# Performance work log

Hardware: AMD Instinct MI355X
Metric: run time of the kernel (lower is better)

Reference implementation:

```python
import jax, jax.numpy as jnp
import numpy as np

H, HD = 16, 64
DIM = H * HD
ROT_DIM = 64
ROT_BASE = 10000.0
B, MAXLEN = 4, 2048
SEQLENS = [2048, 1536, 1024, 512]


def setup_inputs() -> dict:
    key = jax.random.key(0)
    k1, k2, k3 = jax.random.split(key, 3)
    total = sum(SEQLENS)
    hidden_states = jax.random.normal(k1, (total, DIM), jnp.float32)
    Wqkv_w = jax.random.normal(k2, (3 * DIM, DIM), jnp.float32) * (DIM ** -0.5)
    Wo_w = jax.random.normal(k3, (DIM, DIM), jnp.float32) * (DIM ** -0.5)
    cu = np.cumsum([0] + SEQLENS).astype(np.int32)
    idx = np.concatenate([b * MAXLEN + np.arange(L) for b, L in enumerate(SEQLENS)]).astype(np.int64)
    mask = np.zeros((B, MAXLEN), np.int32)
    for b, L in enumerate(SEQLENS):
        mask[b, :L] = 1
    return {"hidden_states": hidden_states, "Wqkv_w": Wqkv_w, "Wo_w": Wo_w,
            "cu_seqlens": jnp.asarray(cu), "indices": jnp.asarray(idx),
            "attn_mask": jnp.asarray(mask), "max_seqlen": MAXLEN}


def _rope(x, positions):
    # x: (B, S, H, D). Non-interleaved (rotate-half) RoPE over first ROT_DIM dims,
    # matching flash_attn RotaryEmbedding(interleaved=False, scale_base=None).
    d2 = ROT_DIM // 2
    inv_freq = 1.0 / (ROT_BASE ** (jnp.arange(0, ROT_DIM, 2, dtype=jnp.float32) / ROT_DIM))
    freqs = positions[:, None].astype(jnp.float32) * inv_freq[None, :]  # (S, d2)
    cos = jnp.cos(freqs)[None, :, None, :]
    sin = jnp.sin(freqs)[None, :, None, :]
    x1, x2 = x[..., :d2], x[..., d2:ROT_DIM]
    rot = jnp.concatenate([x1 * cos - x2 * sin, x2 * cos + x1 * sin], axis=-1)
    if ROT_DIM < x.shape[-1]:
        rot = jnp.concatenate([rot, x[..., ROT_DIM:]], axis=-1)
    return rot


def reference(hidden_states, Wqkv_w, Wo_w, cu_seqlens, indices, attn_mask, max_seqlen):
    # QKV projection on unpadded tokens (no bias: attn_qkv_bias=False)
    qkv = hidden_states @ Wqkv_w.T  # (nnz, 3*dim)
    # pad_input: scatter tokens into (B*max_seqlen) padded layout
    padded = jnp.zeros((B * max_seqlen, 3 * DIM), qkv.dtype).at[indices].set(qkv)
    qkv = padded.reshape(B, max_seqlen, 3, H, HD)
    pos = jnp.arange(max_seqlen)
    q = _rope(qkv[:, :, 0], pos)  # (B, S, H, HD)
    k = _rope(qkv[:, :, 1], pos)
    v = qkv[:, :, 2]
    # SDPA (no attn_mask, matching the source's non-flash path; p_dropout=0)
    scale = 1.0 / jnp.sqrt(jnp.float32(HD))
    scores = jnp.einsum('bqhd,bkhd->bhqk', q, k) * scale  # (B, H, S, S)
    probs = jax.nn.softmax(scores, axis=-1)
    attn = jnp.einsum('bhqk,bkhd->bqhd', probs, v).reshape(B * max_seqlen, DIM)
    # unpad_input_only: gather valid tokens back
    attn = attn[indices]  # (nnz, dim)
    return attn @ Wo_w.T  # attn_out_bias=False, out_drop=Identity
```

## Files before the change

### kernel.cpp

```cpp
#include <hip/hip_runtime.h>
#include <math.h>

#define NH 16
#define HD 64
#define DIM 1024
#define QKV_DIM 3072
#define MAXLEN 2048
#define TOTAL 5120

typedef unsigned short ushort_t;
typedef unsigned int uint_t;
typedef __attribute__((ext_vector_type(8))) short bf16x8;
typedef __attribute__((ext_vector_type(8))) unsigned short ushort8;
typedef __attribute__((ext_vector_type(4))) float f32x4;

__device__ __constant__ int g_cu[5]  = {0, 2048, 3584, 4608, 5120};
__device__ __constant__ int g_seq[4] = {2048, 1536, 1024, 512};

__device__ inline ushort_t f2bf(float f) {
    uint_t u = __float_as_uint(f);
    uint_t r = u + 0x7FFFu + ((u >> 16) & 1u);
    return (ushort_t)(r >> 16);
}
__device__ inline float bf2f(ushort_t h) { return __uint_as_float(((uint_t)h) << 16); }

__global__ __launch_bounds__(256) void split_bf16(const float* __restrict__ x,
                                                  ushort_t* __restrict__ hi,
                                                  ushort_t* __restrict__ lo, int n4) {
    int i = blockIdx.x * 256 + threadIdx.x;
    if (i >= n4) return;
    float4 v = ((const float4*)x)[i];
    ushort_t h0 = f2bf(v.x), h1 = f2bf(v.y), h2 = f2bf(v.z), h3 = f2bf(v.w);
    ushort_t l0 = f2bf(v.x - bf2f(h0));
    ushort_t l1 = f2bf(v.y - bf2f(h1));
    ushort_t l2 = f2bf(v.z - bf2f(h2));
    ushort_t l3 = f2bf(v.w - bf2f(h3));
    ushort4 hv = {h0, h1, h2, h3};
    ushort4 lv = {l0, l1, l2, l3};
    ((ushort4*)hi)[i] = hv;
    ((ushort4*)lo)[i] = lv;
}

__global__ __launch_bounds__(256) void gemm_mfma_split(
    const ushort_t* __restrict__ Ah, const ushort_t* __restrict__ Al,
    const ushort_t* __restrict__ Bh, const ushort_t* __restrict__ Bl,
    float* __restrict__ C, int M, int N, int K) {
    __shared__ ushort_t sAh[128 * 32], sAl[128 * 32];
    __shared__ ushort_t sBh[128 * 32], sBl[128 * 32];

    const int tid = threadIdx.x;
    const int lane = tid & 63;
    const int w = tid >> 6;
    const int bm = blockIdx.y * 128, bn = blockIdx.x * 128;
    const int wm = (w >> 1) * 64, wn = (w & 1) * 64;

    f32x4 acc[4][4] = {};

    const int srow = tid >> 2;
    const int scol = (tid & 3) * 8;

    for (int k0 = 0; k0 < K; k0 += 32) {
        __syncthreads();
#pragma unroll
        for (int i = 0; i < 2; ++i) {
            int r = i * 64 + srow;
            size_t ga = (size_t)(bm + r) * K + k0 + scol;
            size_t gb = (size_t)(bn + r) * K + k0 + scol;
            int ls = r * 32 + scol;
            *(ushort8*)&sAh[ls] = *(const ushort8*)&Ah[ga];
            *(ushort8*)&sAl[ls] = *(const ushort8*)&Al[ga];
            *(ushort8*)&sBh[ls] = *(const ushort8*)&Bh[gb];
            *(ushort8*)&sBl[ls] = *(const ushort8*)&Bl[gb];
        }
        __syncthreads();

        const int frow = lane & 15;
        const int fk = (lane >> 4) * 8;
        bf16x8 ah[4], al[4], bh[4], bl[4];
#pragma unroll
        for (int t = 0; t < 4; ++t) {
            int ar = (wm + t * 16 + frow) * 32 + fk;
            int br = (wn + t * 16 + frow) * 32 + fk;
            ah[t] = *(const bf16x8*)&sAh[ar];
            al[t] = *(const bf16x8*)&sAl[ar];
            bh[t] = *(const bf16x8*)&sBh[br];
            bl[t] = *(const bf16x8*)&sBl[br];
        }
#pragma unroll
        for (int mt = 0; mt < 4; ++mt)
#pragma unroll
            for (int nt = 0; nt < 4; ++nt) {
                acc[mt][nt] = __builtin_amdgcn_mfma_f32_16x16x32_bf16(ah[mt], bh[nt], acc[mt][nt], 0, 0, 0);
                acc[mt][nt] = __builtin_amdgcn_mfma_f32_16x16x32_bf16(ah[mt], bl[nt], acc[mt][nt], 0, 0, 0);
                acc[mt][nt] = __builtin_amdgcn_mfma_f32_16x16x32_bf16(al[mt], bh[nt], acc[mt][nt], 0, 0, 0);
            }
    }

    const int crow0 = (lane >> 4) * 4;
    const int ccol = lane & 15;
#pragma unroll
    for (int mt = 0; mt < 4; ++mt)
#pragma unroll
        for (int nt = 0; nt < 4; ++nt) {
            size_t rbase = (size_t)(bm + wm + mt * 16 + crow0) * N + bn + wn + nt * 16 + ccol;
#pragma unroll
            for (int r = 0; r < 4; ++r)
                C[rbase + (size_t)r * N] = acc[mt][nt][r];
        }
}

__global__ __launch_bounds__(256) void rope_split_kv(
    const float* __restrict__ qkv,
    ushort_t* __restrict__ kh, ushort_t* __restrict__ kl,
    ushort_t* __restrict__ vth, ushort_t* __restrict__ vtl) {
    __shared__ float tv[64][65];

    const int tiles_pref[5] = {0, 32, 56, 72, 80};
    int t = blockIdx.x;
    int b = 0;
    while (t >= tiles_pref[b + 1]) b++;
    const int t0 = (t - tiles_pref[b]) * 64;
    const int base = g_cu[b];
    const int h = blockIdx.y;
    const int tid = threadIdx.x;

    {
        int r = tid >> 2, jg = tid & 3;
        int tok = base + t0 + r;
        const float* kp = qkv + (size_t)tok * QKV_DIM + DIM + h * HD;
        float x1[8], x2[8];
        *(float4*)&x1[0] = *(const float4*)&kp[8 * jg + 0];
        *(float4*)&x1[4] = *(const float4*)&kp[8 * jg + 4];
        *(float4*)&x2[0] = *(const float4*)&kp[32 + 8 * jg + 0];
        *(float4*)&x2[4] = *(const float4*)&kp[32 + 8 * jg + 4];
        float pos = (float)(t0 + r);
        ushort8 h0v, l0v, h1v, l1v;
#pragma unroll
        for (int jj = 0; jj < 8; ++jj) {
            int j = 8 * jg + jj;
            float invf = powf(10000.0f, -(float)j / 32.0f);
            float sn, cs;
            sincosf(pos * invf, &sn, &cs);
            float y0 = x1[jj] * cs - x2[jj] * sn;
            float y1 = x2[jj] * cs + x1[jj] * sn;
            ushort_t hh = f2bf(y0);
            h0v[jj] = hh; l0v[jj] = f2bf(y0 - bf2f(hh));
            hh = f2bf(y1);
            h1v[jj] = hh; l1v[jj] = f2bf(y1 - bf2f(hh));
        }
        size_t o0 = (size_t)tok * DIM + h * HD + 8 * jg;
        *(ushort8*)&kh[o0] = h0v;      *(ushort8*)&kh[o0 + 32] = h1v;
        *(ushort8*)&kl[o0] = l0v;      *(ushort8*)&kl[o0 + 32] = l1v;
    }

#pragma unroll
    for (int it = 0; it < 4; ++it) {
        int item = tid + it * 256;
        int r = item >> 4, c4 = item & 15;
        *(float4*)&tv[r][c4 * 4] =
            *(const float4*)(qkv + (size_t)(base + t0 + r) * QKV_DIM + 2 * DIM + h * HD + c4 * 4);
    }
    __syncthreads();
#pragma unroll
    for (int it = 0; it < 2; ++it) {
        int chunk = tid + it * 256;
        int dd = chunk >> 3, tb = chunk & 7;
        ushort8 vh, vl;
#pragma unroll
        for (int i = 0; i < 8; ++i) {
            float f = tv[tb * 8 + i][dd];
            ushort_t hh = f2bf(f);
            vh[i] = hh; vl[i] = f2bf(f - bf2f(hh));
        }
        size_t off = (size_t)(h * HD + dd) * TOTAL + base + t0 + tb * 8;
        *(ushort8*)&vth[off] = vh;
        *(ushort8*)&vtl[off] = vl;
    }
}

__global__ __launch_bounds__(256) void attn_mfma(
    const float* __restrict__ qkv,
    const ushort_t* __restrict__ kh, const ushort_t* __restrict__ kl,
    const ushort_t* __restrict__ vth, const ushort_t* __restrict__ vtl,
    float* __restrict__ attnb) {
    __shared__ ushort_t sKh[64 * 64], sKl[64 * 64];
    __shared__ ushort_t sVh[64 * 64], sVl[64 * 64];
    __shared__ ushort_t sPh[4][16 * 72], sPl[4][16 * 72];

    const int tiles_pref[5] = {0, 32, 56, 72, 80};
    int t = blockIdx.x;
    int b = 0;
    while (t >= tiles_pref[b + 1]) b++;
    const int qstart = (t - tiles_pref[b]) * 64;
    const int h = blockIdx.y;
    const int L = g_seq[b];
    const int base = g_cu[b];
    const int tid = threadIdx.x;
    const int lane = tid & 63;
    const int w = tid >> 6;
    const int c = lane & 15;
    const int g = lane >> 4;

    const float SCALE = 0.125f * 1.44269504088896f;
    const int qrow = qstart + 16 * w + c;
    const float* qp = qkv + (size_t)(base + qrow) * QKV_DIM + h * HD;
    float x1[8], x2[8];
    *(float4*)&x1[0] = *(const float4*)&qp[8 * g + 0];
    *(float4*)&x1[4] = *(const float4*)&qp[8 * g + 4];
    *(float4*)&x2[0] = *(const float4*)&qp[32 + 8 * g + 0];
    *(float4*)&x2[4] = *(const float4*)&qp[32 + 8 * g + 4];
    bf16x8 qh0, ql0, qh1, ql1;
#pragma unroll
    for (int jj = 0; jj < 8; ++jj) {
        int j = 8 * g + jj;
        float invf = powf(10000.0f, -(float)j / 32.0f);
        float sn, cs;
        sincosf((float)qrow * invf, &sn, &cs);
        float y0 = (x1[jj] * cs - x2[jj] * sn) * SCALE;
        float y1 = (x2[jj] * cs + x1[jj] * sn) * SCALE;
        ushort_t hh = f2bf(y0);
        qh0[jj] = (short)hh; ql0[jj] = (short)f2bf(y0 - bf2f(hh));
        hh = f2bf(y1);
        qh1[jj] = (short)hh; ql1[jj] = (short)f2bf(y1 - bf2f(hh));
    }

    f32x4 o[4] = {};
    float m[4] = {-1e30f, -1e30f, -1e30f, -1e30f};
    float d[4] = {};

    const int ntiles = L >> 6;
    for (int kt = 0; kt < ntiles; ++kt) {
        const int k0 = kt << 6;
        __syncthreads();
#pragma unroll
        for (int it = 0; it < 8; ++it) {
            int chunk = it * 64 + lane;
            int r = chunk >> 3, s = chunk & 7;
            int gb = s ^ (r & 7);
            if (w < 2) {
                const ushort_t* src = (w == 0 ? kh : kl) +
                    (size_t)(base + k0 + r) * DIM + h * HD + 8 * gb;
                ushort8 v = *(const ushort8*)src;
                *(ushort8*)((w == 0 ? sKh : sKl) + r * 64 + 8 * s) = v;
            } else {
                const ushort_t* src = (w == 2 ? vth : vtl) +
                    (size_t)(h * HD + r) * TOTAL + base + k0 + 8 * gb;
                ushort8 v = *(const ushort8*)src;
                *(ushort8*)((w == 2 ? sVh : sVl) + r * 64 + 8 * s) = v;
            }
        }
        __syncthreads();

        f32x4 sf[4] = {};
#pragma unroll
        for (int f = 0; f < 4; ++f) {
#pragma unroll
            for (int ks = 0; ks < 2; ++ks) {
                int off = (16 * f + c) * 64 + 8 * ((4 * ks + g) ^ (c & 7));
                bf16x8 bh = *(const bf16x8*)&sKh[off];
                bf16x8 bl = *(const bf16x8*)&sKl[off];
                bf16x8 qh = ks ? qh1 : qh0;
                bf16x8 ql = ks ? ql1 : ql0;
                sf[f] = __builtin_amdgcn_mfma_f32_16x16x32_bf16(qh, bh, sf[f], 0, 0, 0);
                sf[f] = __builtin_amdgcn_mfma_f32_16x16x32_bf16(qh, bl, sf[f], 0, 0, 0);
                sf[f] = __builtin_amdgcn_mfma_f32_16x16x32_bf16(ql, bh, sf[f], 0, 0, 0);
            }
        }

#pragma unroll
        for (int r = 0; r < 4; ++r) {
            float rm = fmaxf(fmaxf(sf[0][r], sf[1][r]), fmaxf(sf[2][r], sf[3][r]));
            rm = fmaxf(rm, __shfl_xor(rm, 1));
            rm = fmaxf(rm, __shfl_xor(rm, 2));
            rm = fmaxf(rm, __shfl_xor(rm, 4));
            rm = fmaxf(rm, __shfl_xor(rm, 8));
            float mn = fmaxf(m[r], rm);
            float corr = exp2f(m[r] - mn);
            m[r] = mn;
            float p0 = exp2f(sf[0][r] - mn);
            float p1 = exp2f(sf[1][r] - mn);
            float p2 = exp2f(sf[2][r] - mn);
            float p3 = exp2f(sf[3][r] - mn);
            float ps = (p0 + p1) + (p2 + p3);
            ps += __shfl_xor(ps, 1);
            ps += __shfl_xor(ps, 2);
            ps += __shfl_xor(ps, 4);
            ps += __shfl_xor(ps, 8);
            d[r] = d[r] * corr + ps;
            o[0][r] *= corr; o[1][r] *= corr; o[2][r] *= corr; o[3][r] *= corr;
            int ro = (4 * g + r) * 72 + c;
            ushort_t ph;
            ph = f2bf(p0); sPh[w][ro +  0] = ph; sPl[w][ro +  0] = f2bf(p0 - bf2f(ph));
            ph = f2bf(p1); sPh[w][ro + 16] = ph; sPl[w][ro + 16] = f2bf(p1 - bf2f(ph));
            ph = f2bf(p2); sPh[w][ro + 32] = ph; sPl[w][ro + 32] = f2bf(p2 - bf2f(ph));
            ph = f2bf(p3); sPh[w][ro + 48] = ph; sPl[w][ro + 48] = f2bf(p3 - bf2f(ph));
        }
        asm volatile("s_waitcnt lgkmcnt(0)" ::: "memory");
        __builtin_amdgcn_sched_barrier(0);

#pragma unroll
        for (int ks = 0; ks < 2; ++ks) {
            bf16x8 pah = *(const bf16x8*)&sPh[w][c * 72 + 32 * ks + 8 * g];
            bf16x8 pal = *(const bf16x8*)&sPl[w][c * 72 + 32 * ks + 8 * g];
#pragma unroll
            for (int fd = 0; fd < 4; ++fd) {
                int off = (16 * fd + c) * 64 + 8 * ((4 * ks + g) ^ (c & 7));
                bf16x8 vh = *(const bf16x8*)&sVh[off];
                bf16x8 vl = *(const bf16x8*)&sVl[off];
                o[fd] = __builtin_amdgcn_mfma_f32_16x16x32_bf16(pah, vh, o[fd], 0, 0, 0);
                o[fd] = __builtin_amdgcn_mfma_f32_16x16x32_bf16(pah, vl, o[fd], 0, 0, 0);
                o[fd] = __builtin_amdgcn_mfma_f32_16x16x32_bf16(pal, vh, o[fd], 0, 0, 0);
            }
        }
    }

    const int npad = MAXLEN - L;
#pragma unroll
    for (int r = 0; r < 4; ++r) {
        float dr = d[r];
        if (npad) dr += (float)npad * exp2f(0.0f - m[r]);
        float inv = 1.0f / dr;
        int row = base + qstart + 16 * w + 4 * g + r;
        float* op = attnb + (size_t)row * DIM + h * HD;
#pragma unroll
        for (int fd = 0; fd < 4; ++fd)
            op[16 * fd + c] = o[fd][r] * inv;
    }
}

extern "C" void kernel_launch(void* const* d_in, const int* in_sizes, int n_in,
                              void* d_out, int out_size, void* d_ws, size_t ws_size,
                              hipStream_t stream) {
    const float* hidden = (const float*)d_in[0];
    const float* Wqkv = (const float*)d_in[1];
    const float* Wo = (const float*)d_in[2];
    float* out = (float*)d_out;

    const int total = in_sizes[0] / DIM;

    float* qkv = (float*)d_ws;
    float* attnb = qkv + (size_t)total * QKV_DIM;
    ushort_t* us = (ushort_t*)(attnb + (size_t)total * DIM);
    const size_t nh = (size_t)total * DIM;
    const size_t nw = (size_t)QKV_DIM * DIM;
    const size_t no = (size_t)DIM * DIM;
    ushort_t* h_hi = us;            ushort_t* h_lo = h_hi + nh;
    ushort_t* wq_hi = h_lo + nh;    ushort_t* wq_lo = wq_hi + nw;
    ushort_t* ao_hi = wq_lo + nw;   ushort_t* ao_lo = ao_hi + nh;
    ushort_t* wo_hi = ao_lo + nh;   ushort_t* wo_lo = wo_hi + no;
    ushort_t* kh  = h_hi;
    ushort_t* kl  = h_lo;
    ushort_t* vth = wq_hi;
    ushort_t* vtl = ao_hi;

    split_bf16<<<(int)(nh / 4 + 255) / 256, 256, 0, stream>>>(hidden, h_hi, h_lo, (int)(nh / 4));
    split_bf16<<<(int)(nw / 4 + 255) / 256, 256, 0, stream>>>(Wqkv, wq_hi, wq_lo, (int)(nw / 4));
    split_bf16<<<(int)(no / 4 + 255) / 256, 256, 0, stream>>>(Wo, wo_hi, wo_lo, (int)(no / 4));

    gemm_mfma_split<<<dim3(QKV_DIM / 128, total / 128), 256, 0, stream>>>(
        h_hi, h_lo, wq_hi, wq_lo, qkv, total, QKV_DIM, DIM);

    rope_split_kv<<<dim3(80, NH), 256, 0, stream>>>(qkv, kh, kl, vth, vtl);

    attn_mfma<<<dim3(80, NH), 256, 0, stream>>>(qkv, kh, kl, vth, vtl, attnb);

    split_bf16<<<(int)(nh / 4 + 255) / 256, 256, 0, stream>>>(attnb, ao_hi, ao_lo, (int)(nh / 4));
    gemm_mfma_split<<<dim3(DIM / 128, total / 128), 256, 0, stream>>>(
        ao_hi, ao_lo, wo_hi, wo_lo, out, total, DIM, DIM);
}
```

Baseline: 580.5 us.

## Restructure attention kernel: 128-row tiles, register prefetch, lazy rescale, swizzled P

The attention kernel now uses 512-thread blocks covering 128 query rows, so each K/V tile loaded into shared memory is reused by twice as many waves. Next-tile K/V loads are prefetched into registers while the current tile is computed, and all eight waves share the staging work. Softmax skips the max/rescale step unless the row max grows by more than a threshold, and row sums are kept per lane and reduced once at the end. The P scratch buffer is XOR-swizzled instead of padded, and block IDs are remapped across heads. This adds register pressure and a looser numeric bound on the deferred max.

Measured after the change: 707.3 us. +21.8%, slower.

```diff
diff --git a/kernel.cpp b/kernel.cpp
--- a/kernel.cpp
+++ b/kernel.cpp
@@ -178,28 +178,39 @@
     }
 }
 
-__global__ __launch_bounds__(256) void attn_mfma(
+__global__ __launch_bounds__(512, 4) void attn_mfma(
     const float* __restrict__ qkv,
     const ushort_t* __restrict__ kh, const ushort_t* __restrict__ kl,
     const ushort_t* __restrict__ vth, const ushort_t* __restrict__ vtl,
     float* __restrict__ attnb) {
     __shared__ ushort_t sKh[64 * 64], sKl[64 * 64];
     __shared__ ushort_t sVh[64 * 64], sVl[64 * 64];
-    __shared__ ushort_t sPh[4][16 * 72], sPl[4][16 * 72];
-
-    const int tiles_pref[5] = {0, 32, 56, 72, 80};
-    int t = blockIdx.x;
+    __shared__ ushort_t sPh[8][16 * 64], sPl[8][16 * 64];
+
+    int fid = blockIdx.x;
+    fid = (fid & 7) * 80 + (fid >> 3);
+    const int h = fid / 40;
+    int t = fid % 40;
+    const int tiles_pref[5] = {0, 16, 28, 36, 40};
     int b = 0;
     while (t >= tiles_pref[b + 1]) b++;
-    const int qstart = (t - tiles_pref[b]) * 64;
-    const int h = blockIdx.y;
+    const int qstart = (t - tiles_pref[b]) * 128;
     const int L = g_seq[b];
     const int base = g_cu[b];
+
     const int tid = threadIdx.x;
     const int lane = tid & 63;
     const int w = tid >> 6;
     const int c = lane & 15;
     const int g = lane >> 4;
+
+    const int arr = w >> 1;
+    const int half = w & 1;
+    const int l3 = lane >> 3;
+    const int sl = lane & 7;
+    const int gb = sl ^ l3;
+    const ushort_t* gsrc = arr == 0 ? kh : arr == 1 ? kl : arr == 2 ? vth : vtl;
+    ushort_t* ldst = arr == 0 ? sKh : arr == 1 ? sKl : arr == 2 ? sVh : sVl;
 
     const float SCALE = 0.125f * 1.44269504088896f;
     const int qrow = qstart + 16 * w + c;
@@ -226,30 +237,38 @@
 
     f32x4 o[4] = {};
     float m[4] = {-1e30f, -1e30f, -1e30f, -1e30f};
-    float d[4] = {};
+    float dp[4] = {};
+    ushort8 pre[4];
 
     const int ntiles = L >> 6;
+#pragma unroll
+    for (int it = 0; it < 4; ++it) {
+        int rr = half * 32 + it * 8 + l3;
+        size_t src = (arr < 2) ? ((size_t)(base + rr) * DIM + h * HD + 8 * gb)
+                               : ((size_t)(h * HD + rr) * TOTAL + base + 8 * gb);
+        pre[it] = *(const ushort8*)&gsrc[src];
+    }
+
     for (int kt = 0; kt < ntiles; ++kt) {
-        const int k0 = kt << 6;
         __syncthreads();
 #pragma unroll
-        for (int it = 0; it < 8; ++it) {
-            int chunk = it * 64 + lane;
-            int r = chunk >> 3, s = chunk & 7;
-            int gb = s ^ (r & 7);
-            if (w < 2) {
-                const ushort_t* src = (w == 0 ? kh : kl) +
-                    (size_t)(base + k0 + r) * DIM + h * HD + 8 * gb;
-                ushort8 v = *(const ushort8*)src;
-                *(ushort8*)((w == 0 ? sKh : sKl) + r * 64 + 8 * s) = v;
-            } else {
-                const ushort_t* src = (w == 2 ? vth : vtl) +
-                    (size_t)(h * HD + r) * TOTAL + base + k0 + 8 * gb;
-                ushort8 v = *(const ushort8*)src;
-                *(ushort8*)((w == 2 ? sVh : sVl) + r * 64 + 8 * s) = v;
-            }
+        for (int it = 0; it < 4; ++it) {
+            int rr = half * 32 + it * 8 + l3;
+            *(ushort8*)&ldst[rr * 64 + 8 * sl] = pre[it];
         }
         __syncthreads();
+
+        if (kt + 1 < ntiles) {
+            const int k1 = (kt + 1) << 6;
+#pragma unroll
+            for (int it = 0; it < 4; ++it) {
+                int rr = half * 32 + it * 8 + l3;
+                size_t src = (arr < 2)
+                    ? ((size_t)(base + k1 + rr) * DIM + h * HD + 8 * gb)
+                    : ((size_t)(h * HD + rr) * TOTAL + base + k1 + 8 * gb);
+                pre[it] = *(const ushort8*)&gsrc[src];
+            }
+        }
 
         f32x4 sf[4] = {};
 #pragma unroll
@@ -269,39 +288,43 @@
 
 #pragma unroll
         for (int r = 0; r < 4; ++r) {
-            float rm = fmaxf(fmaxf(sf[0][r], sf[1][r]), fmaxf(sf[2][r], sf[3][r]));
-            rm = fmaxf(rm, __shfl_xor(rm, 1));
-            rm = fmaxf(rm, __shfl_xor(rm, 2));
-            rm = fmaxf(rm, __shfl_xor(rm, 4));
-            rm = fmaxf(rm, __shfl_xor(rm, 8));
-            float mn = fmaxf(m[r], rm);
-            float corr = exp2f(m[r] - mn);
-            m[r] = mn;
-            float p0 = exp2f(sf[0][r] - mn);
-            float p1 = exp2f(sf[1][r] - mn);
-            float p2 = exp2f(sf[2][r] - mn);
-            float p3 = exp2f(sf[3][r] - mn);
-            float ps = (p0 + p1) + (p2 + p3);
-            ps += __shfl_xor(ps, 1);
-            ps += __shfl_xor(ps, 2);
-            ps += __shfl_xor(ps, 4);
-            ps += __shfl_xor(ps, 8);
-            d[r] = d[r] * corr + ps;
-            o[0][r] *= corr; o[1][r] *= corr; o[2][r] *= corr; o[3][r] *= corr;
-            int ro = (4 * g + r) * 72 + c;
-            ushort_t ph;
-            ph = f2bf(p0); sPh[w][ro +  0] = ph; sPl[w][ro +  0] = f2bf(p0 - bf2f(ph));
-            ph = f2bf(p1); sPh[w][ro + 16] = ph; sPl[w][ro + 16] = f2bf(p1 - bf2f(ph));
-            ph = f2bf(p2); sPh[w][ro + 32] = ph; sPl[w][ro + 32] = f2bf(p2 - bf2f(ph));
-            ph = f2bf(p3); sPh[w][ro + 48] = ph; sPl[w][ro + 48] = f2bf(p3 - bf2f(ph));
+            float plm = fmaxf(fmaxf(sf[0][r], sf[1][r]), fmaxf(sf[2][r], sf[3][r]));
+            if (!__all(plm <= m[r] + 8.0f)) {
+                float rm = plm;
+                rm = fmaxf(rm, __shfl_xor(rm, 1));
+                rm = fmaxf(rm, __shfl_xor(rm, 2));
+                rm = fmaxf(rm, __shfl_xor(rm, 4));
+                rm = fmaxf(rm, __shfl_xor(rm, 8));
+                float mn = fmaxf(m[r], rm);
+                float corr = exp2f(m[r] - mn);
+                m[r] = mn;
+                dp[r] *= corr;
+                o[0][r] *= corr; o[1][r] *= corr; o[2][r] *= corr; o[3][r] *= corr;
+            }
+            float p0 = exp2f(sf[0][r] - m[r]);
+            float p1 = exp2f(sf[1][r] - m[r]);
+            float p2 = exp2f(sf[2][r] - m[r]);
+            float p3 = exp2f(sf[3][r] - m[r]);
+            dp[r] += (p0 + p1) + (p2 + p3);
+            float pv[4] = {p0, p1, p2, p3};
+            int rbase = (4 * g + r) * 64 + (c & 7);
+            int rx = (4 * g + r) & 7;
+#pragma unroll
+            for (int f = 0; f < 4; ++f) {
+                int addr = rbase + 8 * (((c >> 3) + 2 * f) ^ rx);
+                ushort_t ph = f2bf(pv[f]);
+                sPh[w][addr] = ph;
+                sPl[w][addr] = f2bf(pv[f] - bf2f(ph));
+            }
         }
         asm volatile("s_waitcnt lgkmcnt(0)" ::: "memory");
         __builtin_amdgcn_sched_barrier(0);
 
 #pragma unroll
         for (int ks = 0; ks < 2; ++ks) {
-            bf16x8 pah = *(const bf16x8*)&sPh[w][c * 72 + 32 * ks + 8 * g];
-            bf16x8 pal = *(const bf16x8*)&sPl[w][c * 72 + 32 * ks + 8 * g];
+            int poff = c * 64 + 8 * ((4 * ks + g) ^ (c & 7));
+            bf16x8 pah = *(const bf16x8*)&sPh[w][poff];
+            bf16x8 pal = *(const bf16x8*)&sPl[w][poff];
 #pragma unroll
             for (int fd = 0; fd < 4; ++fd) {
                 int off = (16 * fd + c) * 64 + 8 * ((4 * ks + g) ^ (c & 7));
@@ -317,7 +340,11 @@
     const int npad = MAXLEN - L;
 #pragma unroll
     for (int r = 0; r < 4; ++r) {
-        float dr = d[r];
+        float dr = dp[r];
+        dr += __shfl_xor(dr, 1);
+        dr += __shfl_xor(dr, 2);
+        dr += __shfl_xor(dr, 4);
+        dr += __shfl_xor(dr, 8);
         if (npad) dr += (float)npad * exp2f(0.0f - m[r]);
         float inv = 1.0f / dr;
         int row = base + qstart + 16 * w + 4 * g + r;
@@ -362,7 +389,7 @@
 
     rope_split_kv<<<dim3(80, NH), 256, 0, stream>>>(qkv, kh, kl, vth, vtl);
 
-    attn_mfma<<<dim3(80, NH), 256, 0, stream>>>(qkv, kh, kl, vth, vtl, attnb);
+    attn_mfma<<<640, 512, 0, stream>>>(qkv, kh, kl, vth, vtl, attnb);
 
     split_bf16<<<(int)(nh / 4 + 255) / 256, 256, 0, stream>>>(attnb, ao_hi, ao_lo, (int)(nh / 4));
     gemm_mfma_split<<<dim3(DIM / 128, total / 128), 256, 0, stream>>>(
```
